# Optimization experiments

Hardware: AMD Instinct MI355X
Metric: run time of the kernel (lower is better)

Reference implementation:

```python
import jax, jax.numpy as jnp
import numpy as np

B, S_Q, S_KV = 4, 2048, 2048
D_MODEL, HEADS, D_QK, D_V = 1024, 16, 64, 64


def setup_inputs() -> dict:
    key = jax.random.key(0)
    ks = jax.random.split(key, 12)
    s = lambda fan_in: 1.0 / np.sqrt(fan_in)
    return {
        "x": jax.random.normal(ks[0], (B, S_Q, D_MODEL), jnp.float32),
        "encoder_output": jax.random.normal(ks[1], (B, S_KV, D_MODEL), jnp.float32),
        # per-head Linear weights stacked over heads: [H, D_MODEL, d_head]
        "Wq": jax.random.uniform(ks[2], (HEADS, D_MODEL, D_QK), jnp.float32, -s(D_MODEL), s(D_MODEL)),
        "bq": jax.random.uniform(ks[3], (HEADS, D_QK), jnp.float32, -s(D_MODEL), s(D_MODEL)),
        "Wk": jax.random.uniform(ks[4], (HEADS, D_MODEL, D_QK), jnp.float32, -s(D_MODEL), s(D_MODEL)),
        "bk": jax.random.uniform(ks[5], (HEADS, D_QK), jnp.float32, -s(D_MODEL), s(D_MODEL)),
        "Wv": jax.random.uniform(ks[6], (HEADS, D_MODEL, D_V), jnp.float32, -s(D_MODEL), s(D_MODEL)),
        "bv": jax.random.uniform(ks[7], (HEADS, D_V), jnp.float32, -s(D_MODEL), s(D_MODEL)),
        # output Linear: [H*D_V, D_MODEL]
        "Wo": jax.random.uniform(ks[8], (HEADS * D_V, D_MODEL), jnp.float32, -s(HEADS * D_V), s(HEADS * D_V)),
        "bo": jax.random.uniform(ks[9], (D_MODEL,), jnp.float32, -s(HEADS * D_V), s(HEADS * D_V)),
    }


def reference(x, encoder_output, Wq, bq, Wk, bk, Wv, bv, Wo, bo):
    # Batched equivalent of the per-head Python loop: project all heads at once.
    q = jnp.einsum("bqd,hde->bhqe", x, Wq) + bq[None, :, None, :]              # [B,H,Sq,dk]
    k = jnp.einsum("bsd,hde->bhse", encoder_output, Wk) + bk[None, :, None, :]  # [B,H,Skv,dk]
    v = jnp.einsum("bsd,hde->bhse", encoder_output, Wv) + bv[None, :, None, :]  # [B,H,Skv,dv]
    scale = 1.0 / jnp.sqrt(jnp.asarray(D_QK, x.dtype))
    scores = jnp.einsum("bhqe,bhse->bhqs", q, k) * scale                        # [B,H,Sq,Skv]
    attn = jax.nn.softmax(scores, axis=-1)
    heads = jnp.einsum("bhqs,bhse->bhqe", attn, v)                              # [B,H,Sq,dv]
    # concat heads on last dim (head order matches the torch list concat)
    multihead = heads.transpose(0, 2, 1, 3).reshape(x.shape[0], x.shape[1], HEADS * D_V)
    return multihead @ Wo + bo
```

## Files before the change

### kernel.cpp

```cpp
#include <hip/hip_runtime.h>
#include <hip/hip_bf16.h>
#include <stdint.h>

typedef unsigned short u16;
typedef __bf16 bf16x8 __attribute__((ext_vector_type(8)));
typedef float f32x4 __attribute__((ext_vector_type(4)));
typedef float f32x16 __attribute__((ext_vector_type(16)));
typedef unsigned short us8 __attribute__((ext_vector_type(8)));

__device__ __forceinline__ u16 f2bf(float f) {
  union { float f; uint32_t u; } v; v.f = f;
  uint32_t u = v.u;
  return (u16)((u + 0x7FFFu + ((u >> 16) & 1u)) >> 16);
}

__device__ __forceinline__ uint32_t cvtpk(float a, float b) {
  uint32_t r;
  asm("v_cvt_pk_bf16_f32 %0, %1, %2" : "=v"(r) : "v"(a), "v"(b));
  return r;
}

__device__ __forceinline__ void gload_lds16(const void* g, void* l) {
  __builtin_amdgcn_global_load_lds(
      (const __attribute__((address_space(1))) void*)(uintptr_t)g,
      (__attribute__((address_space(3))) void*)(uint32_t)(uintptr_t)l,
      16, 0, 0);
}

__device__ __forceinline__ float vsum16(f32x16 v) {
  float a = (v[0] + v[1]) + (v[2] + v[3]);
  float b = (v[4] + v[5]) + (v[6] + v[7]);
  float c = (v[8] + v[9]) + (v[10] + v[11]);
  float d = (v[12] + v[13]) + (v[14] + v[15]);
  return (a + b) + (c + d);
}

#define CROW(r, g) (((r) & 3) + 8 * ((r) >> 2) + 4 * (g))

__global__ __launch_bounds__(256) void cvt_all_k(
    const float* __restrict__ x, const float* __restrict__ enc,
    const float* __restrict__ Wq, const float* __restrict__ Wk,
    const float* __restrict__ Wv, const float* __restrict__ Wo,
    u16* __restrict__ xb, u16* __restrict__ eb,
    u16* __restrict__ wqb, u16* __restrict__ wkb,
    u16* __restrict__ wvb, u16* __restrict__ wob) {
  __shared__ float t[64][65];
  const int blk = blockIdx.x;
  const int tid = threadIdx.x;

  if (blk < 8192) {
    const float* in = (blk < 4096) ? x : enc;
    u16* out = (blk < 4096) ? xb : eb;
    size_t i = (size_t)(blk & 4095) * 256 + tid;
    const float4* p = (const float4*)in + i * 2;
    float4 a = p[0], b = p[1];
    us8 o;
    o[0] = f2bf(a.x); o[1] = f2bf(a.y); o[2] = f2bf(a.z); o[3] = f2bf(a.w);
    o[4] = f2bf(b.x); o[5] = f2bf(b.y); o[6] = f2bf(b.z); o[7] = f2bf(b.w);
    *(us8*)(out + i * 8) = o;
    return;
  }

  if (blk < 8960) {
    int r = blk - 8192;
    int z = r >> 8;
    const float* W = (z == 0) ? Wq : (z == 1) ? Wk : Wv;
    u16* o = (z == 0) ? wqb : (z == 1) ? wkb : wvb;
    const int h = (r & 255) >> 4, d0 = (r & 15) * 64;
    const float* Wb = W + ((size_t)h << 16) + (size_t)d0 * 64;
#pragma unroll
    for (int i = 0; i < 4; ++i) {
      int idx = tid + i * 256;
      int dl = idx >> 4, e4 = (idx & 15) << 2;
      float4 v = *(const float4*)(Wb + dl * 64 + e4);
      t[dl][e4 + 0] = v.x; t[dl][e4 + 1] = v.y; t[dl][e4 + 2] = v.z; t[dl][e4 + 3] = v.w;
    }
    __syncthreads();
#pragma unroll
    for (int i = 0; i < 2; ++i) {
      int idx = tid + i * 256;
      int e = idx >> 3, dc = (idx & 7) * 8;
      us8 w;
#pragma unroll
      for (int j = 0; j < 8; ++j) w[j] = f2bf(t[dc + j][e]);
      *(us8*)(o + ((size_t)(h * 64 + e)) * 1024 + d0 + dc) = w;
    }
    return;
  }

  {
    int r = blk - 8960;
    const int k0 = (r & 15) * 64, n0 = (r >> 4) * 64;
    const float* Wb = Wo + (size_t)k0 * 1024 + n0;
#pragma unroll
    for (int i = 0; i < 4; ++i) {
      int idx = tid + i * 256;
      int kl = idx >> 4, n4 = (idx & 15) << 2;
      float4 v = *(const float4*)(Wb + (size_t)kl * 1024 + n4);
      t[kl][n4 + 0] = v.x; t[kl][n4 + 1] = v.y; t[kl][n4 + 2] = v.z; t[kl][n4 + 3] = v.w;
    }
    __syncthreads();
#pragma unroll
    for (int i = 0; i < 2; ++i) {
      int idx = tid + i * 256;
      int n = idx >> 3, kc = (idx & 7) * 8;
      us8 w;
#pragma unroll
      for (int j = 0; j < 8; ++j) w[j] = f2bf(t[kc + j][n]);
      *(us8*)(wob + ((size_t)(n0 + n)) * 1024 + k0 + kc) = w;
    }
  }
}

template <int MODE>
__global__ __launch_bounds__(256) void gemm_bt_k(const u16* __restrict__ A,
                                                 const u16* __restrict__ B,
                                                 const float* __restrict__ bias,
                                                 const float* __restrict__ bias2,
                                                 void* __restrict__ C, void* __restrict__ C2,
                                                 int M, int N, int K, float scale) {
  __shared__ __attribute__((aligned(16))) u16 As[2][128 * 32];
  __shared__ __attribute__((aligned(16))) u16 Bs[2][128 * 32];
  const int tid = threadIdx.x;
  const int wave = tid >> 6, lane = tid & 63;
  const int lo = lane & 15, hi = lane >> 4;
  const int n0 = blockIdx.x * 128, m0 = blockIdx.y * 128;
  const int wr = wave >> 1, wc = wave & 1;

  f32x4 acc[4][4] = {};

  const int o0 = wave * 1024 + lane * 16;
  const int r0 = o0 >> 6, cb0 = o0 & 63;
  const int o1 = o0 + 4096;
  const int r1 = o1 >> 6, cb1 = o1 & 63;

  const char* Ac = (const char*)A;
  const char* Bc = (const char*)B;
  const size_t ksz = (size_t)K * 2;

  auto STAGE = [&](int t) {
    const size_t kb = (size_t)t * 64;
    char* Ad = (char*)As[t & 1];
    char* Bd = (char*)Bs[t & 1];
    gload_lds16(Ac + (size_t)(m0 + r0) * ksz + kb + cb0, Ad + o0);
    gload_lds16(Ac + (size_t)(m0 + r1) * ksz + kb + cb1, Ad + o1);
    gload_lds16(Bc + (size_t)(n0 + r0) * ksz + kb + cb0, Bd + o0);
    gload_lds16(Bc + (size_t)(n0 + r1) * ksz + kb + cb1, Bd + o1);
  };

  const int NK = K >> 5;
  STAGE(0);
  STAGE(1);

  for (int kk = 0; kk < NK; ++kk) {
    if (kk < NK - 1) {
      asm volatile("s_waitcnt vmcnt(4)" ::: "memory");
    } else {
      asm volatile("s_waitcnt vmcnt(0)" ::: "memory");
    }
    __builtin_amdgcn_s_barrier();
    __builtin_amdgcn_sched_barrier(0);
    const u16* Asb = As[kk & 1];
    const u16* Bsb = Bs[kk & 1];
    bf16x8 af[4], bfr[4];
#pragma unroll
    for (int i = 0; i < 4; ++i) {
      af[i]  = *(const bf16x8*)(Asb + (wr * 64 + i * 16 + lo) * 32 + hi * 8);
      bfr[i] = *(const bf16x8*)(Bsb + (wc * 64 + i * 16 + lo) * 32 + hi * 8);
    }
    asm volatile("s_waitcnt lgkmcnt(0)" ::: "memory");
    __builtin_amdgcn_sched_barrier(0);
    __builtin_amdgcn_s_barrier();
    if (kk + 2 < NK) STAGE(kk + 2);
    __builtin_amdgcn_s_setprio(1);
#pragma unroll
    for (int am = 0; am < 4; ++am)
#pragma unroll
      for (int bn = 0; bn < 4; ++bn)
        acc[am][bn] = __builtin_amdgcn_mfma_f32_16x16x32_bf16(af[am], bfr[bn], acc[am][bn], 0, 0, 0);
    __builtin_amdgcn_s_setprio(0);
  }

  if constexpr (MODE == 0) {
    u16* Co = (u16*)C;
#pragma unroll
    for (int bn = 0; bn < 4; ++bn) {
      int col = n0 + wc * 64 + bn * 16 + lo;
      float bb = bias[col];
      int hh = col >> 6, e = col & 63;
#pragma unroll
      for (int am = 0; am < 4; ++am) {
#pragma unroll
        for (int r = 0; r < 4; ++r) {
          int row = m0 + wr * 64 + am * 16 + hi * 4 + r;
          int b = row >> 11, s = row & 2047;
          Co[(((size_t)(b * 16 + hh) * 2048 + s) << 6) + e] = f2bf((acc[am][bn][r] + bb) * scale);
        }
      }
    }
  } else if constexpr (MODE == 1) {
    float* Cf = (float*)C;
#pragma unroll
    for (int bn = 0; bn < 4; ++bn) {
      int col = n0 + wc * 64 + bn * 16 + lo;
      float bb = bias[col];
#pragma unroll
      for (int am = 0; am < 4; ++am) {
#pragma unroll
        for (int r = 0; r < 4; ++r) {
          int row = m0 + wr * 64 + am * 16 + hi * 4 + r;
          Cf[(size_t)row * N + col] = acc[am][bn][r] + bb;
        }
      }
    }
  } else {
    const bool isV = (n0 + wc * 64) >= 1024;
    if (!isV) {
      u16* Co = (u16*)C;
#pragma unroll
      for (int bn = 0; bn < 4; ++bn) {
        int col = n0 + wc * 64 + bn * 16 + lo;
        float bb = bias[col];
        int hh = col >> 6, e = col & 63;
#pragma unroll
        for (int am = 0; am < 4; ++am) {
#pragma unroll
          for (int r = 0; r < 4; ++r) {
            int row = m0 + wr * 64 + am * 16 + hi * 4 + r;
            int b = row >> 11, s = row & 2047;
            s = (s & ~12) | ((s & 4) << 1) | ((s & 8) >> 1);
            Co[(((size_t)(b * 16 + hh) * 2048 + s) << 6) + e] = f2bf(acc[am][bn][r] + bb);
          }
        }
      }
    } else {
      u16* Vt = (u16*)C2;
#pragma unroll
      for (int bn = 0; bn < 4; ++bn) {
        int c = (n0 + wc * 64 + bn * 16 + lo) - 1024;
        float bb = bias2[c];
        int hh = c >> 6, e = c & 63;
#pragma unroll
        for (int am = 0; am < 4; ++am) {
          int row = m0 + wr * 64 + am * 16 + hi * 4;
          int b = row >> 11, s = row & 2047;
          uint2 wv;
          wv.x = cvtpk(acc[am][bn][0] + bb, acc[am][bn][1] + bb);
          wv.y = cvtpk(acc[am][bn][2] + bb, acc[am][bn][3] + bb);
          *(uint2*)(Vt + (((size_t)(b * 16 + hh) * 64 + e) * 2048 + s)) = wv;
        }
      }
    }
  }
}

__global__ __launch_bounds__(256, 4) void attn_k(const u16* __restrict__ Qg,
                                                 const u16* __restrict__ Kg,
                                                 const u16* __restrict__ Vtg,
                                                 u16* __restrict__ Hd) {
  const int W = blockIdx.x;
  const int bid = (W >> 7) * 128 + (W & 7) * 16 + ((W >> 3) & 15);
  const int bh = bid >> 4;
  const int q0 = (bid & 15) * 128;
  const int tid = threadIdx.x;
  const int w = tid >> 6, lane = tid & 63;
  const int q31 = lane & 31, g = lane >> 5;

  __shared__ __attribute__((aligned(16))) char LB[2][16384];

  bf16x8 qf0, qf1, qf2, qf3;
  {
    const char* Qrow = (const char*)(Qg + ((size_t)bh * 2048 + q0 + w * 32 + q31) * 64) + g * 16;
    qf0 = *(const bf16x8*)(Qrow);
    qf1 = *(const bf16x8*)(Qrow + 32);
    qf2 = *(const bf16x8*)(Qrow + 64);
    qf3 = *(const bf16x8*)(Qrow + 96);
  }

  f32x16 acc0 = {}, acc1 = {};
  float lrun = 0.f;

  const int lrow = lane >> 3;
  const int scol = ((lane & 7) ^ lrow) << 4;
  const char* kp = (const char*)Kg + (size_t)bh * 262144 + (size_t)(w * 16 + lrow) * 128 + scol;
  const char* vp = (const char*)Vtg + (size_t)bh * 262144 + (size_t)(w * 16 + lrow) * 4096 + scol;

  auto STAGE = [&](int c) {
    char* kb = &LB[c][0] + w * 2048;
    char* vb = kb + 8192;
    gload_lds16(kp, kb);
    gload_lds16(kp + 1024, kb + 1024);
    gload_lds16(vp, vb);
    gload_lds16(vp + 32768, vb + 1024);
    kp += 8192;
    vp += 128;
  };

  STAGE(0);

  const int swz = (q31 & 7) << 4;
  const int krow = q31 * 128;
  const int ko0 = (g * 16) ^ swz;
  const int ko1 = (32 + g * 16) ^ swz;
  const int ko2 = (64 + g * 16) ^ swz;
  const int ko3 = (96 + g * 16) ^ swz;

  int cur = 0;
  for (int t = 0; t < 32; ++t) {
    asm volatile("s_waitcnt vmcnt(0)" ::: "memory");
    __builtin_amdgcn_s_barrier();
    asm volatile("" ::: "memory");
    if (t < 31) STAGE(cur ^ 1);

    const char* Kc = &LB[cur][0];
    const char* Vc = Kc + 8192;

    f32x16 p0 = {}, p1 = {};
    __builtin_amdgcn_s_setprio(1);
    {
      bf16x8 kf;
      kf = *(const bf16x8*)(Kc + krow + ko0);
      p0 = __builtin_amdgcn_mfma_f32_32x32x16_bf16(kf, qf0, p0, 0, 0, 0);
      kf = *(const bf16x8*)(Kc + 4096 + krow + ko0);
      p1 = __builtin_amdgcn_mfma_f32_32x32x16_bf16(kf, qf0, p1, 0, 0, 0);
      kf = *(const bf16x8*)(Kc + krow + ko1);
      p0 = __builtin_amdgcn_mfma_f32_32x32x16_bf16(kf, qf1, p0, 0, 0, 0);
      kf = *(const bf16x8*)(Kc + 4096 + krow + ko1);
      p1 = __builtin_amdgcn_mfma_f32_32x32x16_bf16(kf, qf1, p1, 0, 0, 0);
      kf = *(const bf16x8*)(Kc + krow + ko2);
      p0 = __builtin_amdgcn_mfma_f32_32x32x16_bf16(kf, qf2, p0, 0, 0, 0);
      kf = *(const bf16x8*)(Kc + 4096 + krow + ko2);
      p1 = __builtin_amdgcn_mfma_f32_32x32x16_bf16(kf, qf2, p1, 0, 0, 0);
      kf = *(const bf16x8*)(Kc + krow + ko3);
      p0 = __builtin_amdgcn_mfma_f32_32x32x16_bf16(kf, qf3, p0, 0, 0, 0);
      kf = *(const bf16x8*)(Kc + 4096 + krow + ko3);
      p1 = __builtin_amdgcn_mfma_f32_32x32x16_bf16(kf, qf3, p1, 0, 0, 0);
    }
    __builtin_amdgcn_s_setprio(0);

#pragma unroll
    for (int i = 0; i < 16; ++i) p0[i] = __builtin_amdgcn_exp2f(p0[i]);
#pragma unroll
    for (int i = 0; i < 16; ++i) p1[i] = __builtin_amdgcn_exp2f(p1[i]);

    float rs = vsum16(p0) + vsum16(p1);
    {
      float ra = rs, rb = rs;
      asm("v_permlane32_swap_b32 %0, %1" : "+v"(ra), "+v"(rb));
      rs += g ? ra : rb;
    }
    lrun += rs;

    union PU { uint32_t u[4]; bf16x8 v; } a0, a1, a2, a3;
    a0.u[0] = cvtpk(p0[0], p0[1]);   a0.u[1] = cvtpk(p0[2], p0[3]);
    a0.u[2] = cvtpk(p0[4], p0[5]);   a0.u[3] = cvtpk(p0[6], p0[7]);
    a1.u[0] = cvtpk(p0[8], p0[9]);   a1.u[1] = cvtpk(p0[10], p0[11]);
    a1.u[2] = cvtpk(p0[12], p0[13]); a1.u[3] = cvtpk(p0[14], p0[15]);
    a2.u[0] = cvtpk(p1[0], p1[1]);   a2.u[1] = cvtpk(p1[2], p1[3]);
    a2.u[2] = cvtpk(p1[4], p1[5]);   a2.u[3] = cvtpk(p1[6], p1[7]);
    a3.u[0] = cvtpk(p1[8], p1[9]);   a3.u[1] = cvtpk(p1[10], p1[11]);
    a3.u[2] = cvtpk(p1[12], p1[13]); a3.u[3] = cvtpk(p1[14], p1[15]);

    __builtin_amdgcn_s_setprio(1);
    {
      bf16x8 vf;
      vf = *(const bf16x8*)(Vc + krow + ko0);
      acc0 = __builtin_amdgcn_mfma_f32_32x32x16_bf16(a0.v, vf, acc0, 0, 0, 0);
      vf = *(const bf16x8*)(Vc + 4096 + krow + ko0);
      acc1 = __builtin_amdgcn_mfma_f32_32x32x16_bf16(a0.v, vf, acc1, 0, 0, 0);
      vf = *(const bf16x8*)(Vc + krow + ko1);
      acc0 = __builtin_amdgcn_mfma_f32_32x32x16_bf16(a1.v, vf, acc0, 0, 0, 0);
      vf = *(const bf16x8*)(Vc + 4096 + krow + ko1);
      acc1 = __builtin_amdgcn_mfma_f32_32x32x16_bf16(a1.v, vf, acc1, 0, 0, 0);
      vf = *(const bf16x8*)(Vc + krow + ko2);
      acc0 = __builtin_amdgcn_mfma_f32_32x32x16_bf16(a2.v, vf, acc0, 0, 0, 0);
      vf = *(const bf16x8*)(Vc + 4096 + krow + ko2);
      acc1 = __builtin_amdgcn_mfma_f32_32x32x16_bf16(a2.v, vf, acc1, 0, 0, 0);
      vf = *(const bf16x8*)(Vc + krow + ko3);
      acc0 = __builtin_amdgcn_mfma_f32_32x32x16_bf16(a3.v, vf, acc0, 0, 0, 0);
      vf = *(const bf16x8*)(Vc + 4096 + krow + ko3);
      acc1 = __builtin_amdgcn_mfma_f32_32x32x16_bf16(a3.v, vf, acc1, 0, 0, 0);
    }
    __builtin_amdgcn_s_setprio(0);

    cur ^= 1;
  }

  float linv = 1.f / lrun;
  const int b = bh >> 4, h = bh & 15;
  u16* Ho = Hd + ((size_t)b * 2048 + q0 + w * 32) * 1024 + h * 64;
#pragma unroll
  for (int r = 0; r < 16; ++r) {
    float iv = __shfl(linv, CROW(r, g));
    int q = CROW(r, g);
    u16* row = Ho + (size_t)q * 1024;
    row[q31]      = f2bf(acc0[r] * iv);
    row[32 + q31] = f2bf(acc1[r] * iv);
  }
}


extern "C" void kernel_launch(void* const* d_in, const int* in_sizes, int n_in,
                              void* d_out, int out_size, void* d_ws, size_t ws_size,
                              hipStream_t stream) {
  const float* x   = (const float*)d_in[0];
  const float* enc = (const float*)d_in[1];
  const float* Wq  = (const float*)d_in[2];
  const float* bq  = (const float*)d_in[3];
  const float* Wk  = (const float*)d_in[4];
  const float* bk  = (const float*)d_in[5];
  const float* Wv  = (const float*)d_in[6];
  const float* bv  = (const float*)d_in[7];
  const float* Wo  = (const float*)d_in[8];
  const float* bo  = (const float*)d_in[9];
  float* out = (float*)d_out;
  char* ws = (char*)d_ws;

  const size_t SZ = 16u * 1024u * 1024u;
  u16* xb  = (u16*)(ws + 0 * SZ);
  u16* eb  = (u16*)(ws + 1 * SZ);
  u16* Qg  = (u16*)(ws + 2 * SZ);
  u16* Kg  = (u16*)(ws + 3 * SZ);
  u16* vtb = (u16*)(ws + 4 * SZ);
  u16* wqb = (u16*)(ws + 5 * SZ + 0u * (2u << 20));
  u16* wkb = (u16*)(ws + 5 * SZ + 1u * (2u << 20));
  u16* wvb = (u16*)(ws + 5 * SZ + 2u * (2u << 20));
  u16* wob = (u16*)(ws + 5 * SZ + 3u * (2u << 20));
  u16* hd  = xb;

  const float cs = 0.18033688011112042f;

  cvt_all_k<<<9216, 256, 0, stream>>>(x, enc, Wq, Wk, Wv, Wo, xb, eb, wqb, wkb, wvb, wob);

  gemm_bt_k<0><<<dim3(8, 64), 256, 0, stream>>>(xb, wqb, bq, nullptr, Qg, nullptr,
                                                8192, 1024, 1024, cs);
  gemm_bt_k<2><<<dim3(16, 64), 256, 0, stream>>>(eb, wkb, bk, bv, Kg, vtb,
                                                 8192, 2048, 1024, 1.0f);

  attn_k<<<1024, 256, 0, stream>>>(Qg, Kg, vtb, hd);

  gemm_bt_k<1><<<dim3(8, 64), 256, 0, stream>>>(hd, wob, bo, nullptr, out, nullptr,
                                                8192, 1024, 1024, 1.0f);
}
```

Baseline: 201.7 us.

## Merge Q and KV projections into one launch, triple-buffer attention K/V staging

The Q projection and the fused K/V projection now run as a single kernel over a 1536-block grid that branches on block index. This removes one launch boundary and lets the two GEMMs fill the GPU together. The attention kernel moves from double to triple buffering of K/V tiles in LDS, prefetching two tiles ahead with a partial vmcnt wait. The extra LDS forces occupancy down from 4 to 3 blocks per CU.

```diff
diff --git a/kernel.cpp b/kernel.cpp
--- a/kernel.cpp
+++ b/kernel.cpp
@@ -112,36 +112,23 @@
   }
 }
 
-template <int MODE>
-__global__ __launch_bounds__(256) void gemm_bt_k(const u16* __restrict__ A,
-                                                 const u16* __restrict__ B,
-                                                 const float* __restrict__ bias,
-                                                 const float* __restrict__ bias2,
-                                                 void* __restrict__ C, void* __restrict__ C2,
-                                                 int M, int N, int K, float scale) {
-  __shared__ __attribute__((aligned(16))) u16 As[2][128 * 32];
-  __shared__ __attribute__((aligned(16))) u16 Bs[2][128 * 32];
-  const int tid = threadIdx.x;
+__device__ __forceinline__ void gemm_core(const char* Ac, const char* Bc, int K,
+                                          int m0, int n0, int tid,
+                                          char* As0, char* As1, char* Bs0, char* Bs1,
+                                          f32x4 (&acc)[4][4]) {
   const int wave = tid >> 6, lane = tid & 63;
   const int lo = lane & 15, hi = lane >> 4;
-  const int n0 = blockIdx.x * 128, m0 = blockIdx.y * 128;
   const int wr = wave >> 1, wc = wave & 1;
-
-  f32x4 acc[4][4] = {};
-
   const int o0 = wave * 1024 + lane * 16;
   const int r0 = o0 >> 6, cb0 = o0 & 63;
   const int o1 = o0 + 4096;
   const int r1 = o1 >> 6, cb1 = o1 & 63;
-
-  const char* Ac = (const char*)A;
-  const char* Bc = (const char*)B;
   const size_t ksz = (size_t)K * 2;
 
   auto STAGE = [&](int t) {
     const size_t kb = (size_t)t * 64;
-    char* Ad = (char*)As[t & 1];
-    char* Bd = (char*)Bs[t & 1];
+    char* Ad = (t & 1) ? As1 : As0;
+    char* Bd = (t & 1) ? Bs1 : Bs0;
     gload_lds16(Ac + (size_t)(m0 + r0) * ksz + kb + cb0, Ad + o0);
     gload_lds16(Ac + (size_t)(m0 + r1) * ksz + kb + cb1, Ad + o1);
     gload_lds16(Bc + (size_t)(n0 + r0) * ksz + kb + cb0, Bd + o0);
@@ -160,8 +147,8 @@
     }
     __builtin_amdgcn_s_barrier();
     __builtin_amdgcn_sched_barrier(0);
-    const u16* Asb = As[kk & 1];
-    const u16* Bsb = Bs[kk & 1];
+    const u16* Asb = (const u16*)((kk & 1) ? As1 : As0);
+    const u16* Bsb = (const u16*)((kk & 1) ? Bs1 : Bs0);
     bf16x8 af[4], bfr[4];
 #pragma unroll
     for (int i = 0; i < 4; ++i) {
@@ -180,13 +167,32 @@
         acc[am][bn] = __builtin_amdgcn_mfma_f32_16x16x32_bf16(af[am], bfr[bn], acc[am][bn], 0, 0, 0);
     __builtin_amdgcn_s_setprio(0);
   }
-
-  if constexpr (MODE == 0) {
-    u16* Co = (u16*)C;
+}
+
+__global__ __launch_bounds__(256) void qkv_proj_k(
+    const u16* __restrict__ xb, const u16* __restrict__ eb,
+    const u16* __restrict__ wqb, const u16* __restrict__ wkvb,
+    const float* __restrict__ bq, const float* __restrict__ bk_,
+    const float* __restrict__ bv_,
+    u16* __restrict__ Qg, u16* __restrict__ Kg, u16* __restrict__ Vt, float scale) {
+  __shared__ __attribute__((aligned(16))) char As[2][8192];
+  __shared__ __attribute__((aligned(16))) char Bs[2][8192];
+  const int blk = blockIdx.x;
+  const int tid = threadIdx.x;
+  const int wave = tid >> 6, lane = tid & 63;
+  const int lo = lane & 15, hi = lane >> 4;
+  const int wr = wave >> 1, wc = wave & 1;
+
+  f32x4 acc[4][4] = {};
+
+  if (blk < 512) {
+    const int n0 = (blk & 7) * 128, m0 = (blk >> 3) * 128;
+    gemm_core((const char*)xb, (const char*)wqb, 1024, m0, n0, tid,
+              As[0], As[1], Bs[0], Bs[1], acc);
 #pragma unroll
     for (int bn = 0; bn < 4; ++bn) {
       int col = n0 + wc * 64 + bn * 16 + lo;
-      float bb = bias[col];
+      float bb = bq[col];
       int hh = col >> 6, e = col & 63;
 #pragma unroll
       for (int am = 0; am < 4; ++am) {
@@ -194,33 +200,21 @@
         for (int r = 0; r < 4; ++r) {
           int row = m0 + wr * 64 + am * 16 + hi * 4 + r;
           int b = row >> 11, s = row & 2047;
-          Co[(((size_t)(b * 16 + hh) * 2048 + s) << 6) + e] = f2bf((acc[am][bn][r] + bb) * scale);
+          Qg[(((size_t)(b * 16 + hh) * 2048 + s) << 6) + e] = f2bf((acc[am][bn][r] + bb) * scale);
         }
       }
     }
-  } else if constexpr (MODE == 1) {
-    float* Cf = (float*)C;
-#pragma unroll
-    for (int bn = 0; bn < 4; ++bn) {
-      int col = n0 + wc * 64 + bn * 16 + lo;
-      float bb = bias[col];
-#pragma unroll
-      for (int am = 0; am < 4; ++am) {
-#pragma unroll
-        for (int r = 0; r < 4; ++r) {
-          int row = m0 + wr * 64 + am * 16 + hi * 4 + r;
-          Cf[(size_t)row * N + col] = acc[am][bn][r] + bb;
-        }
-      }
-    }
   } else {
+    const int r_ = blk - 512;
+    const int n0 = (r_ & 15) * 128, m0 = (r_ >> 4) * 128;
+    gemm_core((const char*)eb, (const char*)wkvb, 1024, m0, n0, tid,
+              As[0], As[1], Bs[0], Bs[1], acc);
     const bool isV = (n0 + wc * 64) >= 1024;
     if (!isV) {
-      u16* Co = (u16*)C;
 #pragma unroll
       for (int bn = 0; bn < 4; ++bn) {
         int col = n0 + wc * 64 + bn * 16 + lo;
-        float bb = bias[col];
+        float bb = bk_[col];
         int hh = col >> 6, e = col & 63;
 #pragma unroll
         for (int am = 0; am < 4; ++am) {
@@ -229,16 +223,15 @@
             int row = m0 + wr * 64 + am * 16 + hi * 4 + r;
             int b = row >> 11, s = row & 2047;
             s = (s & ~12) | ((s & 4) << 1) | ((s & 8) >> 1);
-            Co[(((size_t)(b * 16 + hh) * 2048 + s) << 6) + e] = f2bf(acc[am][bn][r] + bb);
+            Kg[(((size_t)(b * 16 + hh) * 2048 + s) << 6) + e] = f2bf(acc[am][bn][r] + bb);
           }
         }
       }
     } else {
-      u16* Vt = (u16*)C2;
 #pragma unroll
       for (int bn = 0; bn < 4; ++bn) {
         int c = (n0 + wc * 64 + bn * 16 + lo) - 1024;
-        float bb = bias2[c];
+        float bb = bv_[c];
         int hh = c >> 6, e = c & 63;
 #pragma unroll
         for (int am = 0; am < 4; ++am) {
@@ -254,7 +247,38 @@
   }
 }
 
-__global__ __launch_bounds__(256, 4) void attn_k(const u16* __restrict__ Qg,
+__global__ __launch_bounds__(256) void out_proj_k(const u16* __restrict__ A,
+                                                  const u16* __restrict__ B,
+                                                  const float* __restrict__ bias,
+                                                  float* __restrict__ C, int M, int N, int K) {
+  __shared__ __attribute__((aligned(16))) char As[2][8192];
+  __shared__ __attribute__((aligned(16))) char Bs[2][8192];
+  const int tid = threadIdx.x;
+  const int wave = tid >> 6, lane = tid & 63;
+  const int lo = lane & 15, hi = lane >> 4;
+  const int wr = wave >> 1, wc = wave & 1;
+  const int n0 = blockIdx.x * 128, m0 = blockIdx.y * 128;
+
+  f32x4 acc[4][4] = {};
+  gemm_core((const char*)A, (const char*)B, K, m0, n0, tid,
+            As[0], As[1], Bs[0], Bs[1], acc);
+
+#pragma unroll
+  for (int bn = 0; bn < 4; ++bn) {
+    int col = n0 + wc * 64 + bn * 16 + lo;
+    float bb = bias[col];
+#pragma unroll
+    for (int am = 0; am < 4; ++am) {
+#pragma unroll
+      for (int r = 0; r < 4; ++r) {
+        int row = m0 + wr * 64 + am * 16 + hi * 4 + r;
+        C[(size_t)row * N + col] = acc[am][bn][r] + bb;
+      }
+    }
+  }
+}
+
+__global__ __launch_bounds__(256, 3) void attn_k(const u16* __restrict__ Qg,
                                                  const u16* __restrict__ Kg,
                                                  const u16* __restrict__ Vtg,
                                                  u16* __restrict__ Hd) {
@@ -266,7 +290,7 @@
   const int w = tid >> 6, lane = tid & 63;
   const int q31 = lane & 31, g = lane >> 5;
 
-  __shared__ __attribute__((aligned(16))) char LB[2][16384];
+  __shared__ __attribute__((aligned(16))) char LB[3][16384];
 
   bf16x8 qf0, qf1, qf2, qf3;
   {
@@ -297,6 +321,7 @@
   };
 
   STAGE(0);
+  STAGE(1);
 
   const int swz = (q31 & 7) << 4;
   const int krow = q31 * 128;
@@ -305,14 +330,18 @@
   const int ko2 = (64 + g * 16) ^ swz;
   const int ko3 = (96 + g * 16) ^ swz;
 
-  int cur = 0;
+  int bc = 0;
   for (int t = 0; t < 32; ++t) {
-    asm volatile("s_waitcnt vmcnt(0)" ::: "memory");
+    if (t < 31) {
+      asm volatile("s_waitcnt vmcnt(4)" ::: "memory");
+    } else {
+      asm volatile("s_waitcnt vmcnt(0)" ::: "memory");
+    }
     __builtin_amdgcn_s_barrier();
     asm volatile("" ::: "memory");
-    if (t < 31) STAGE(cur ^ 1);
-
-    const char* Kc = &LB[cur][0];
+    if (t < 30) STAGE(bc == 0 ? 2 : bc - 1);
+
+    const char* Kc = &LB[bc][0];
     const char* Vc = Kc + 8192;
 
     f32x16 p0 = {}, p1 = {};
@@ -383,7 +412,7 @@
     }
     __builtin_amdgcn_s_setprio(0);
 
-    cur ^= 1;
+    bc = (bc == 2) ? 0 : bc + 1;
   }
 
   float linv = 1.f / lrun;
@@ -424,21 +453,17 @@
   u16* vtb = (u16*)(ws + 4 * SZ);
   u16* wqb = (u16*)(ws + 5 * SZ + 0u * (2u << 20));
   u16* wkb = (u16*)(ws + 5 * SZ + 1u * (2u << 20));
-  u16* wvb = (u16*)(ws + 5 * SZ + 2u * (2u << 20));
   u16* wob = (u16*)(ws + 5 * SZ + 3u * (2u << 20));
   u16* hd  = xb;
 
   const float cs = 0.18033688011112042f;
 
-  cvt_all_k<<<9216, 256, 0, stream>>>(x, enc, Wq, Wk, Wv, Wo, xb, eb, wqb, wkb, wvb, wob);
-
-  gemm_bt_k<0><<<dim3(8, 64), 256, 0, stream>>>(xb, wqb, bq, nullptr, Qg, nullptr,
-                                                8192, 1024, 1024, cs);
-  gemm_bt_k<2><<<dim3(16, 64), 256, 0, stream>>>(eb, wkb, bk, bv, Kg, vtb,
-                                                 8192, 2048, 1024, 1.0f);
+  cvt_all_k<<<9216, 256, 0, stream>>>(x, enc, Wq, Wk, Wv, Wo, xb, eb, wqb, wkb,
+                                      (u16*)(ws + 5 * SZ + 2u * (2u << 20)), wob);
+
+  qkv_proj_k<<<1536, 256, 0, stream>>>(xb, eb, wqb, wkb, bq, bk, bv, Qg, Kg, vtb, cs);
 
   attn_k<<<1024, 256, 0, stream>>>(Qg, Kg, vtb, hd);
 
-  gemm_bt_k<1><<<dim3(8, 64), 256, 0, stream>>>(hd, wob, bo, nullptr, out, nullptr,
-                                                8192, 1024, 1024, 1.0f);
-}
+  out_proj_k<<<dim3(8, 64), 256, 0, stream>>>(hd, wob, bo, out, 8192, 1024, 1024);
+}
```

Result: faster. 193.6 us (-4.0%).
